# Optimization experiments

Hardware: AMD Instinct MI355X
Metric: run time of the kernel (lower is better)

Reference implementation:

```python
import jax, jax.numpy as jnp
import numpy as np

B, N, V, H, R, A, IN, K = 64, 512, 64, 512, 4, 18, 128, 32
EPS = 1e-8


def setup_inputs() -> dict:
    key = jax.random.key(0)
    ks = jax.random.split(key, 20)
    g = lambda i, shape, s=1.0: jax.random.normal(ks[i], shape, jnp.float32) * s
    u = lambda i, shape: jax.random.uniform(ks[i], shape, dtype=jnp.float32)
    cin = IN + R * V
    return dict(
        x=g(0, (B, IN)),
        h=g(1, (B, H), 0.1),
        c=g(2, (B, H), 0.1),
        memory=g(3, (B, N, V), 0.1),
        read_weights=u(4, (B, R, N)),
        write_weights=u(5, (B, N)),
        usage=u(6, (B, N)),
        link_matrix=u(7, (B, N, N)) * 0.01,
        precedence_weights=u(8, (B, N)),
        W_ih=g(9, (4 * H, cin), 0.05), W_hh=g(10, (4 * H, H), 0.05),
        b_ih=jnp.zeros(4 * H, jnp.float32), b_hh=jnp.zeros(4 * H, jnp.float32),
        W_read=g(11, (R, V + 4, H), 0.05), b_read=jnp.zeros((R, V + 4), jnp.float32),
        W_write=g(12, (3 * V + 3, H), 0.05), b_write=jnp.zeros(3 * V + 3, jnp.float32),
        W_pol=g(13, (A, H), 0.05), b_pol=jnp.zeros(A, jnp.float32),
        W_val=g(14, (1, H), 0.05), b_val=jnp.zeros(1, jnp.float32),
    )


def reference(x, h, c, memory, read_weights, write_weights, usage, link_matrix,
              precedence_weights, W_ih, W_hh, b_ih, b_hh, W_read, b_read,
              W_write, b_write, W_pol, b_pol, W_val, b_val):
    # ---- read heads (vectorized over R) ----
    ro = jnp.einsum('roh,bh->bro', W_read, h) + b_read            # [B,R,V+4]
    rkey = ro[..., :V]
    rbeta = jax.nn.softplus(ro[..., V])                           # [B,R]
    rpi = jax.nn.softmax(ro[..., V + 1:V + 4], axis=-1)           # backward/content/forward gates
    mem_norm = jnp.maximum(jnp.linalg.norm(memory, axis=-1), EPS)  # [B,N]
    key_norm = jnp.maximum(jnp.linalg.norm(rkey, axis=-1), EPS)    # [B,R]
    sim = jnp.einsum('bnv,brv->brn', memory, rkey) / (mem_norm[:, None, :] * key_norm[..., None])
    scores = rbeta[..., None] * sim                                # [B,R,N]
    kth = jax.lax.top_k(scores, K)[0][..., -1:]                    # sparse top-k mask
    cw = jax.nn.softmax(jnp.where(scores >= kth, scores, -jnp.inf), axis=-1)
    fw = jnp.einsum('bnm,brm->brn', link_matrix, read_weights)     # forward weighting L w
    bw = jnp.einsum('bmn,brm->brn', link_matrix, read_weights)     # backward weighting L^T w
    w_r = rpi[..., 0:1] * bw + rpi[..., 1:2] * cw + rpi[..., 2:3] * fw  # [B,R,N]
    rvec = jnp.einsum('brn,bnv->brv', w_r, memory).reshape(B, R * V)
    # ---- LSTM controller (torch LSTMCell gate order i,f,g,o) ----
    gates = jnp.concatenate([x, rvec], -1) @ W_ih.T + h @ W_hh.T + b_ih + b_hh
    i_g, f_g, g_g, o_g = jnp.split(gates, 4, axis=-1)
    c_new = jax.nn.sigmoid(f_g) * c + jax.nn.sigmoid(i_g) * jnp.tanh(g_g)
    h_new = jax.nn.sigmoid(o_g) * jnp.tanh(c_new)
    # ---- write head ----
    wo = h_new @ W_write.T + b_write                               # [B,3V+3]
    wkey = wo[:, :V]
    erase = jax.nn.sigmoid(wo[:, V:2 * V])
    add = jnp.tanh(wo[:, 2 * V:3 * V])
    wbeta = jax.nn.softplus(wo[:, 3 * V])
    g_a = jax.nn.sigmoid(wo[:, 3 * V + 1])
    g_w = jax.nn.sigmoid(wo[:, 3 * V + 2])
    wkey_norm = jnp.maximum(jnp.linalg.norm(wkey, axis=-1), EPS)
    wsim = jnp.einsum('bnv,bv->bn', memory, wkey) / (mem_norm * wkey_norm[:, None])
    cw_w = jax.nn.softmax(wbeta[:, None] * wsim, axis=-1)
    # allocation weighting from sorted usage (DNC Eq. 1)
    idx = jnp.argsort(usage, axis=-1)
    u_sorted = jnp.take_along_axis(usage, idx, -1)
    prod_prev = jnp.concatenate([jnp.ones((B, 1), usage.dtype), jnp.cumprod(u_sorted, -1)[:, :-1]], -1)
    a_sorted = (1.0 - u_sorted) * prod_prev
    alloc = jnp.take_along_axis(a_sorted, jnp.argsort(idx, -1), -1)
    write_w = g_w[:, None] * (g_a[:, None] * alloc + (1.0 - g_a)[:, None] * cw_w)  # [B,N]
    # ---- memory erase/add ----
    mem_new = memory * (1.0 - write_w[:, :, None] * erase[:, None, :]) + write_w[:, :, None] * add[:, None, :]
    # ---- usage (psi detached as in torch.no_grad) ----
    psi = jax.lax.stop_gradient(jnp.prod(1.0 - w_r, axis=1))
    usage_new = (usage + write_weights - usage * write_weights) * psi
    # ---- link matrix + precedence ----
    ws = jnp.sum(write_w, -1, keepdims=True)
    prec_new = (1.0 - ws) * precedence_weights + write_w
    decay = (1.0 - write_w[:, :, None]) * (1.0 - write_w[:, None, :])
    link_new = decay * link_matrix + write_w[:, :, None] * precedence_weights[:, None, :]
    link_new = link_new * (1.0 - jnp.eye(N, dtype=link_new.dtype))
    # ---- actor/critic heads ----
    logits = h_new @ W_pol.T + b_pol
    value = h_new @ W_val.T + b_val
    return (logits, value, h_new, c_new, mem_new, w_r, write_w, usage_new, link_new, prec_new)
```

## Files before the change

### kernel.cpp

```cpp
#include <hip/hip_runtime.h>
#include <math.h>

constexpr int Bb = 64, Nn = 512, Vv = 64, Hh = 512, Rr = 4, Aa = 18, INp = 128, KTOP = 32;
constexpr int CIN = 384;
constexpr int WOUT = 195;
#define EPSf 1e-8f

__device__ __forceinline__ float sigmoidf(float x){ return 1.f/(1.f+expf(-x)); }
__device__ __forceinline__ float softplusf(float x){ return (x>20.f)? x : log1pf(expf(x)); }
__device__ __forceinline__ float wave_reduce(float v){
  #pragma unroll
  for(int o=32;o>0;o>>=1) v += __shfl_down(v, o, 64);
  return v;
}
__device__ __forceinline__ unsigned f2ord(float f){
  unsigned u = __float_as_uint(f);
  return (u & 0x80000000u) ? ~u : (u | 0x80000000u);
}

__global__ void k_stage1(const float* __restrict__ link, const float* __restrict__ rw,
                         const float* __restrict__ Wr, const float* __restrict__ brd,
                         const float* __restrict__ h,
                         float* __restrict__ fw, float* __restrict__ bwpart,
                         float* __restrict__ rvec,
                         float* __restrict__ ro, float* __restrict__ rp) {
  __shared__ float bl[4][4][512];
  __shared__ float sh[512];
  __shared__ float sro[68];
  if (blockIdx.x < 512) {
    if (blockIdx.x < 64) rvec[blockIdx.x*256 + threadIdx.x] = 0.f;
    int b  = blockIdx.x >> 3;
    int ch = blockIdx.x & 7;
    int wv = threadIdx.x >> 6, lane = threadIdx.x & 63;
    const float* rwb = rw + b*Rr*Nn;
    float rwv[4][8];
    #pragma unroll
    for (int r = 0; r < 4; ++r)
      #pragma unroll
      for (int t = 0; t < 8; ++t) rwv[r][t] = rwb[r*512 + lane + 64*t];
    float bwacc[8][4] = {};
    const float* lb = link + (size_t)b*Nn*Nn;
    int n0 = ch*64 + wv*16;
    for (int i = 0; i < 16; ++i) {
      int n = n0 + i;
      float lk[8];
      #pragma unroll
      for (int t = 0; t < 8; ++t) lk[t] = lb[n*512 + lane + 64*t];
      float s0 = rwb[n], s1 = rwb[512+n], s2 = rwb[1024+n], s3 = rwb[1536+n];
      float f0=0,f1=0,f2=0,f3=0;
      #pragma unroll
      for (int t = 0; t < 8; ++t) {
        float lv = lk[t];
        f0 += lv*rwv[0][t]; f1 += lv*rwv[1][t]; f2 += lv*rwv[2][t]; f3 += lv*rwv[3][t];
        bwacc[t][0] += lv*s0; bwacc[t][1] += lv*s1; bwacc[t][2] += lv*s2; bwacc[t][3] += lv*s3;
      }
      f0 = wave_reduce(f0); f1 = wave_reduce(f1);
      f2 = wave_reduce(f2); f3 = wave_reduce(f3);
      if (lane == 0) {
        fw[(b*Rr+0)*Nn+n] = f0; fw[(b*Rr+1)*Nn+n] = f1;
        fw[(b*Rr+2)*Nn+n] = f2; fw[(b*Rr+3)*Nn+n] = f3;
      }
    }
    #pragma unroll
    for (int t = 0; t < 8; ++t)
      #pragma unroll
      for (int r = 0; r < 4; ++r) bl[wv][r][lane + 64*t] = bwacc[t][r];
    __syncthreads();
    int tid = threadIdx.x;
    #pragma unroll
    for (int q = 0; q < 8; ++q) {
      int idx = q*256 + tid;
      int r = idx >> 9, j = idx & 511;
      float v = bl[0][r][j] + bl[1][r][j] + bl[2][r][j] + bl[3][r][j];
      bwpart[((size_t)(ch*Bb + b)*Rr + r)*Nn + j] = v;
    }
  } else {
    int blk = blockIdx.x - 512;
    int b = blk >> 2, r = blk & 3;
    int wv = threadIdx.x >> 6, lane = threadIdx.x & 63;
    const float* hb = h + b*Hh;
    for (int i = threadIdx.x; i < 512; i += 256) sh[i] = hb[i];
    __syncthreads();
    const float* wbase = Wr + (size_t)(r*68)*Hh;
    for (int q = 0; q < 17; ++q) {
      int p = wv*17 + q;
      const float* wrow = wbase + (size_t)p*Hh;
      float acc = 0.f;
      #pragma unroll
      for (int t = 0; t < 8; ++t) { int k = lane + 64*t; acc += wrow[k]*sh[k]; }
      acc = wave_reduce(acc);
      if (lane == 0) sro[p] = acc + brd[r*68 + p];
    }
    __syncthreads();
    if (threadIdx.x < 68) ro[b*272 + r*68 + threadIdx.x] = sro[threadIdx.x];
    if (wv == 0) {
      float kv = sro[lane];
      float k2 = wave_reduce(kv*kv);
      if (lane == 0) {
        float rbeta = softplusf(sro[64]);
        float sc = rbeta / fmaxf(sqrtf(k2), EPSf);
        float e0 = sro[65], e1 = sro[66], e2 = sro[67];
        float mm = fmaxf(e0, fmaxf(e1, e2));
        float x0 = expf(e0-mm), x1 = expf(e1-mm), x2 = expf(e2-mm);
        float inv = 1.f/(x0+x1+x2);
        float* rpb = rp + (b*4 + r)*4;
        rpb[0] = sc; rpb[1] = x0*inv; rpb[2] = x1*inv; rpb[3] = x2*inv;
      }
    }
  }
}

__global__ void k_scores(const float* __restrict__ mem, const float* __restrict__ ro,
                         const float* __restrict__ rp, float* __restrict__ scores,
                         float* __restrict__ invmn) {
  int row = blockIdx.x*4 + (threadIdx.x>>6);
  int lane = threadIdx.x & 63;
  int b = row >> 9, n = row & 511;
  float m = mem[row*Vv + lane];
  const float* rob = ro + b*272;
  float v0 = m*m;
  float v1 = m * rob[lane];
  float v2 = m * rob[68  + lane];
  float v3 = m * rob[136 + lane];
  float v4 = m * rob[204 + lane];
  #pragma unroll
  for (int o = 32; o > 0; o >>= 1) {
    v0 += __shfl_down(v0,o,64); v1 += __shfl_down(v1,o,64);
    v2 += __shfl_down(v2,o,64); v3 += __shfl_down(v3,o,64);
    v4 += __shfl_down(v4,o,64);
  }
  if (lane == 0) {
    float im = 1.f / fmaxf(sqrtf(v0), EPSf);
    invmn[row] = im;
    const float* rpb = rp + b*16;
    scores[(b*4+0)*Nn+n] = rpb[0]  * v1 * im;
    scores[(b*4+1)*Nn+n] = rpb[4]  * v2 * im;
    scores[(b*4+2)*Nn+n] = rpb[8]  * v3 * im;
    scores[(b*4+3)*Nn+n] = rpb[12] * v4 * im;
  }
}

__global__ void k_topk_cw(const float* __restrict__ scores, float* __restrict__ cw) {
  __shared__ unsigned long long sk[512];
  __shared__ float sred[4];
  __shared__ float skv[2];
  int br = blockIdx.x, tid = threadIdx.x;
  float v0 = scores[br*Nn + tid], v1 = scores[br*Nn + tid + 256];
  unsigned long long k0 = ((unsigned long long)f2ord(v0) << 32) | (unsigned)(511 - tid);
  unsigned long long k1 = ((unsigned long long)f2ord(v1) << 32) | (unsigned)(255 - tid);
  sk[tid] = k0; sk[tid+256] = k1;
  __syncthreads();
  int c0 = 0, c1 = 0;
  #pragma unroll 8
  for (int j = 0; j < 512; ++j) {
    unsigned long long kj = sk[j];
    c0 += (kj > k0); c1 += (kj > k1);
  }
  if (c0 == KTOP-1) skv[0] = v0;
  if (c1 == KTOP-1) skv[0] = v1;
  if (c0 == 0) skv[1] = v0;
  if (c1 == 0) skv[1] = v1;
  __syncthreads();
  float kth = skv[0], mx = skv[1];
  float e0 = (v0 >= kth) ? expf(v0-mx) : 0.f;
  float e1 = (v1 >= kth) ? expf(v1-mx) : 0.f;
  float s = wave_reduce(e0+e1);
  if ((tid&63) == 0) sred[tid>>6] = s;
  __syncthreads();
  float inv = 1.f/(sred[0]+sred[1]+sred[2]+sred[3]);
  cw[br*Nn+tid]     = e0*inv;
  cw[br*Nn+tid+256] = e1*inv;
}

__global__ void k_wrrv(const float* __restrict__ bwpart, const float* __restrict__ cw,
                       const float* __restrict__ fw, const float* __restrict__ rp,
                       const float* __restrict__ usage, const float* __restrict__ wwt,
                       const float* __restrict__ mem,
                       float* __restrict__ out_wr, float* __restrict__ out_usage,
                       float* __restrict__ rvec) {
  __shared__ float swr[4][256];
  int b = blockIdx.x >> 1, ch = blockIdx.x & 1;
  int tid = threadIdx.x;
  int n = ch*256 + tid;
  int idx = b*Nn + n;
  float psi = 1.f;
  #pragma unroll
  for (int r = 0; r < 4; ++r) {
    int brr = b*4 + r;
    float bwv = 0.f;
    #pragma unroll
    for (int chh = 0; chh < 8; ++chh)
      bwv += bwpart[((size_t)(chh*Bb + b)*Rr + r)*Nn + n];
    const float* rpb = rp + brr*4;
    float w = rpb[1]*bwv + rpb[2]*cw[brr*Nn+n] + rpb[3]*fw[brr*Nn+n];
    out_wr[brr*Nn+n] = w;
    swr[r][tid] = w;
    psi *= (1.f - w);
  }
  float u = usage[idx], wt = wwt[idx];
  out_usage[idx] = (u + wt - u*wt) * psi;
  __syncthreads();
  int r = tid >> 6, v = tid & 63;
  const float* mb = mem + ((size_t)b*Nn + ch*256)*Vv + v;
  float acc = 0.f;
  #pragma unroll 4
  for (int t = 0; t < 256; ++t) acc += swr[r][t] * mb[t*Vv];
  atomicAdd(&rvec[(b*4+r)*Vv + v], acc);
}

__global__ void k_gates_lstm(const float* __restrict__ x, const float* __restrict__ rvec,
                             const float* __restrict__ h, const float* __restrict__ Wih,
                             const float* __restrict__ Whh, const float* __restrict__ bih,
                             const float* __restrict__ bhh, const float* __restrict__ c,
                             float* __restrict__ out_h, float* __restrict__ out_c) {
  int gid = blockIdx.x*4 + (threadIdx.x>>6);
  int lane = threadIdx.x & 63;
  int hh = gid >> 4;
  int bt = gid & 15;
  float acc[4][4] = {};
  #pragma unroll
  for (int t = 0; t < 6; ++t) {
    int k = lane + 64*t;
    float u[4], w[4];
    #pragma unroll
    for (int i = 0; i < 4; ++i) {
      int b = bt*4 + i;
      u[i] = (k < INp) ? x[b*INp + k] : rvec[b*(Rr*Vv) + k - INp];
      w[i] = Wih[(size_t)(i*Hh + hh)*CIN + k];
    }
    #pragma unroll
    for (int g = 0; g < 4; ++g)
      #pragma unroll
      for (int bb = 0; bb < 4; ++bb) acc[g][bb] += w[g]*u[bb];
  }
  #pragma unroll
  for (int t = 0; t < 8; ++t) {
    int k = lane + 64*t;
    float u[4], w[4];
    #pragma unroll
    for (int i = 0; i < 4; ++i) {
      u[i] = h[(bt*4+i)*Hh + k];
      w[i] = Whh[(size_t)(i*Hh + hh)*Hh + k];
    }
    #pragma unroll
    for (int g = 0; g < 4; ++g)
      #pragma unroll
      for (int bb = 0; bb < 4; ++bb) acc[g][bb] += w[g]*u[bb];
  }
  #pragma unroll
  for (int g = 0; g < 4; ++g)
    #pragma unroll
    for (int bb = 0; bb < 4; ++bb) acc[g][bb] = wave_reduce(acc[g][bb]);
  if (lane == 0) {
    float bsum[4];
    #pragma unroll
    for (int g = 0; g < 4; ++g) bsum[g] = bih[g*Hh + hh] + bhh[g*Hh + hh];
    #pragma unroll
    for (int bb = 0; bb < 4; ++bb) {
      int b = bt*4 + bb;
      float ig = sigmoidf(acc[0][bb] + bsum[0]);
      float fg = sigmoidf(acc[1][bb] + bsum[1]);
      float gg = tanhf   (acc[2][bb] + bsum[2]);
      float og = sigmoidf(acc[3][bb] + bsum[3]);
      float cn = fg * c[b*Hh + hh] + ig * gg;
      float hn = og * tanhf(cn);
      out_c[b*Hh + hh] = cn;
      out_h[b*Hh + hh] = hn;
    }
  }
}

__global__ void k_wopol(const float* __restrict__ hn, const float* __restrict__ Ww,
                        const float* __restrict__ bw_, const float* __restrict__ Wp,
                        const float* __restrict__ bp, const float* __restrict__ Wv,
                        const float* __restrict__ bv, float* __restrict__ wo,
                        float* __restrict__ out_logits, float* __restrict__ out_value) {
  int gid = blockIdx.x*4 + (threadIdx.x>>6);
  int lane = threadIdx.x & 63;
  int b = gid / 214, o = gid % 214;
  const float* wrow;
  if (o < WOUT) wrow = Ww + o*Hh;
  else if (o < WOUT + Aa) wrow = Wp + (o-WOUT)*Hh;
  else wrow = Wv;
  const float* hb = hn + b*Hh;
  float acc = 0.f;
  #pragma unroll
  for (int t = 0; t < 8; ++t) { int k = lane+64*t; acc += hb[k]*wrow[k]; }
  acc = wave_reduce(acc);
  if (lane == 0) {
    if (o < WOUT) wo[b*WOUT+o] = acc + bw_[o];
    else if (o < WOUT + Aa) out_logits[b*Aa + (o-WOUT)] = acc + bp[o-WOUT];
    else out_value[b] = acc + bv[0];
  }
}

__global__ void k_wsim(const float* __restrict__ mem, const float* __restrict__ wo,
                       const float* __restrict__ invmn, float* __restrict__ wsim) {
  int row = blockIdx.x*4 + (threadIdx.x>>6);
  int lane = threadIdx.x & 63;
  int b = row >> 9;
  const float* wob = wo + b*WOUT;
  float kv = wob[lane];
  float m = mem[row*Vv + lane];
  float v0 = m*kv, v1 = kv*kv;
  #pragma unroll
  for (int o = 32; o > 0; o >>= 1) {
    v0 += __shfl_down(v0,o,64); v1 += __shfl_down(v1,o,64);
  }
  if (lane == 0) {
    float wbeta = softplusf(wob[192]);
    wsim[row] = wbeta * v0 * invmn[row] / fmaxf(sqrtf(v1), EPSf);
  }
}

__global__ void k_alloc(const float* __restrict__ usage, const float* __restrict__ wo,
                        const float* __restrict__ wsim, const float* __restrict__ prec,
                        float* __restrict__ out_ww, float* __restrict__ out_prec) {
  __shared__ unsigned long long sk[512];
  __shared__ float su[512];
  __shared__ float cp[512];
  __shared__ float sred[8];
  int b = blockIdx.x, tid = threadIdx.x;
  int wv = tid >> 6, lane = tid & 63;
  float s0 = wsim[b*Nn+tid], s1 = wsim[b*Nn+tid+256];
  float u0 = usage[b*Nn+tid], u1 = usage[b*Nn+tid+256];
  unsigned long long k0 = ((unsigned long long)f2ord(u0) << 32) | (unsigned)tid;
  unsigned long long k1 = ((unsigned long long)f2ord(u1) << 32) | (unsigned)(tid+256);
  sk[tid] = k0; sk[tid+256] = k1;
  float mxl = fmaxf(s0, s1);
  #pragma unroll
  for (int o = 32; o > 0; o >>= 1) mxl = fmaxf(mxl, __shfl_down(mxl,o,64));
  if (lane == 0) sred[wv] = mxl;
  __syncthreads();
  float mx = fmaxf(fmaxf(sred[0],sred[1]), fmaxf(sred[2],sred[3]));
  float e0 = expf(s0-mx), e1 = expf(s1-mx);
  float ssum = wave_reduce(e0+e1);
  if (lane == 0) sred[4+wv] = ssum;
  int r0 = 0, r1 = 0;
  #pragma unroll 8
  for (int j = 0; j < 512; ++j) {
    unsigned long long kj = sk[j];
    r0 += (kj < k0); r1 += (kj < k1);
  }
  __syncthreads();
  float cinv = 1.f/(sred[4]+sred[5]+sred[6]+sred[7]);
  float c0 = e0*cinv, c1 = e1*cinv;
  su[r0] = u0; su[r1] = u1;
  __syncthreads();
  cp[tid] = su[tid]; cp[tid+256] = su[tid+256];
  __syncthreads();
  for (int d = 1; d < 512; d <<= 1) {
    float t0 = cp[tid]     * ((tid >= d)     ? cp[tid-d]     : 1.f);
    float t1 = cp[tid+256] * ((tid+256 >= d) ? cp[tid+256-d] : 1.f);
    __syncthreads();
    cp[tid] = t0; cp[tid+256] = t1;
    __syncthreads();
  }
  float pp0 = (r0 == 0) ? 1.f : cp[r0-1];
  float pp1 = (r1 == 0) ? 1.f : cp[r1-1];
  float a0 = (1.f-u0)*pp0, a1 = (1.f-u1)*pp1;
  float ga = sigmoidf(wo[b*WOUT+193]);
  float gw = sigmoidf(wo[b*WOUT+194]);
  float wv0 = gw * (ga*a0 + (1.f-ga)*c0);
  float wv1 = gw * (ga*a1 + (1.f-ga)*c1);
  out_ww[b*Nn+tid]     = wv0;
  out_ww[b*Nn+tid+256] = wv1;
  float ws_ = wave_reduce(wv0+wv1);
  if (lane == 0) sred[wv] = ws_;
  __syncthreads();
  float wsum = sred[0]+sred[1]+sred[2]+sred[3];
  out_prec[b*Nn+tid]     = (1.f-wsum)*prec[b*Nn+tid]     + wv0;
  out_prec[b*Nn+tid+256] = (1.f-wsum)*prec[b*Nn+tid+256] + wv1;
}

__global__ void k_memlink(const float* __restrict__ link, const float* __restrict__ ww,
                          const float* __restrict__ prec, const float* __restrict__ mem,
                          const float* __restrict__ wo, float* __restrict__ out_link,
                          float* __restrict__ out_mem) {
  int bid = blockIdx.x;
  if (bid < 16384) {
    int idx4 = bid*256 + threadIdx.x;
    int base = idx4*4;
    int b = base >> 18;
    int rem = base & 262143;
    int i = rem >> 9;
    int j0 = rem & 511;
    float wi = ww[b*Nn + i];
    float fi = 1.f - wi;
    float4 lv = *(const float4*)(link + base);
    float4 wj = *(const float4*)(ww + b*Nn + j0);
    float4 pj = *(const float4*)(prec + b*Nn + j0);
    float4 o;
    o.x = fi*(1.f-wj.x)*lv.x + wi*pj.x;
    o.y = fi*(1.f-wj.y)*lv.y + wi*pj.y;
    o.z = fi*(1.f-wj.z)*lv.z + wi*pj.z;
    o.w = fi*(1.f-wj.w)*lv.w + wi*pj.w;
    if (i >= j0 && i < j0+4) {
      if (i == j0) o.x = 0.f;
      else if (i == j0+1) o.y = 0.f;
      else if (i == j0+2) o.z = 0.f;
      else o.w = 0.f;
    }
    *(float4*)(out_link + base) = o;
  } else {
    int idx4 = (bid - 16384)*256 + threadIdx.x;
    int base = idx4*4;
    int b = base >> 15;
    int rem = base & 32767;
    int n = rem >> 6;
    int v0 = rem & 63;
    float w = ww[b*Nn + n];
    const float* wob = wo + b*WOUT;
    float4 m = *(const float4*)(mem + base);
    float4 o;
    float e, a;
    e = sigmoidf(wob[64+v0+0]); a = tanhf(wob[128+v0+0]); o.x = m.x*(1.f-w*e)+w*a;
    e = sigmoidf(wob[64+v0+1]); a = tanhf(wob[128+v0+1]); o.y = m.y*(1.f-w*e)+w*a;
    e = sigmoidf(wob[64+v0+2]); a = tanhf(wob[128+v0+2]); o.z = m.z*(1.f-w*e)+w*a;
    e = sigmoidf(wob[64+v0+3]); a = tanhf(wob[128+v0+3]); o.w = m.w*(1.f-w*e)+w*a;
    *(float4*)(out_mem + base) = o;
  }
}

extern "C" void kernel_launch(void* const* d_in, const int* in_sizes, int n_in,
                              void* d_out, int out_size, void* d_ws, size_t ws_size,
                              hipStream_t stream) {
  const float* x    = (const float*)d_in[0];
  const float* h    = (const float*)d_in[1];
  const float* c    = (const float*)d_in[2];
  const float* mem  = (const float*)d_in[3];
  const float* rw   = (const float*)d_in[4];
  const float* wwt  = (const float*)d_in[5];
  const float* usage= (const float*)d_in[6];
  const float* link = (const float*)d_in[7];
  const float* prec = (const float*)d_in[8];
  const float* Wih  = (const float*)d_in[9];
  const float* Whh  = (const float*)d_in[10];
  const float* bih  = (const float*)d_in[11];
  const float* bhh  = (const float*)d_in[12];
  const float* Wr   = (const float*)d_in[13];
  const float* br   = (const float*)d_in[14];
  const float* Ww   = (const float*)d_in[15];
  const float* bw_  = (const float*)d_in[16];
  const float* Wp   = (const float*)d_in[17];
  const float* bp   = (const float*)d_in[18];
  const float* Wv   = (const float*)d_in[19];
  const float* bv   = (const float*)d_in[20];

  float* out = (float*)d_out;
  float* o_logits = out + 0;
  float* o_value  = out + 1152;
  float* o_h      = out + 1216;
  float* o_c      = out + 33984;
  float* o_mem    = out + 66752;
  float* o_wr     = out + 2163904;
  float* o_ww     = out + 2294976;
  float* o_usage  = out + 2327744;
  float* o_link   = out + 2360512;
  float* o_prec   = out + 19137728;

  float* ws = (float*)d_ws;
  float* ws_ro     = ws;
  float* ws_rp     = ws + 17408;
  float* ws_sc     = ws + 18432;
  float* ws_cw     = ws + 149504;
  float* ws_fw     = ws + 280576;
  float* ws_bwpart = ws + 411648;
  float* ws_rvec   = ws + 1460224;
  float* ws_wo     = ws + 1476608;
  float* ws_wsim   = ws + 1489088;
  float* ws_invmn  = ws + 1521856;

  k_stage1     <<<dim3(768),       dim3(256), 0, stream>>>(link, rw, Wr, br, h, ws_fw, ws_bwpart, ws_rvec, ws_ro, ws_rp);
  k_scores     <<<dim3(Bb*Nn/4),   dim3(256), 0, stream>>>(mem, ws_ro, ws_rp, ws_sc, ws_invmn);
  k_topk_cw    <<<dim3(Bb*Rr),     dim3(256), 0, stream>>>(ws_sc, ws_cw);
  k_wrrv       <<<dim3(Bb*2),      dim3(256), 0, stream>>>(ws_bwpart, ws_cw, ws_fw, ws_rp, usage, wwt, mem, o_wr, o_usage, ws_rvec);
  k_gates_lstm <<<dim3(2048),      dim3(256), 0, stream>>>(x, ws_rvec, h, Wih, Whh, bih, bhh, c, o_h, o_c);
  k_wopol      <<<dim3(Bb*214/4),  dim3(256), 0, stream>>>(o_h, Ww, bw_, Wp, bp, Wv, bv, ws_wo, o_logits, o_value);
  k_wsim       <<<dim3(Bb*Nn/4),   dim3(256), 0, stream>>>(mem, ws_wo, ws_invmn, ws_wsim);
  k_alloc      <<<dim3(Bb),        dim3(256), 0, stream>>>(usage, ws_wo, ws_wsim, prec, o_ww, o_prec);
  k_memlink    <<<dim3(16384+2048),dim3(256), 0, stream>>>(link, o_ww, prec, mem, ws_wo, o_link, o_mem);
}
```

Measured before the change: 296.3 us.

## Fuse scores/top-k into stage1 and merge write-head kernels into one tail

Content-similarity scoring and sparse top-k softmax now run inside the read-head blocks of k_stage1, which compute the key and then score all 512 memory rows in place. The write-projection/policy/value matvec, the write similarity and the allocation logic are merged into a single per-batch k_tail kernel, cutting nine launches to five and dropping several intermediate buffers. The read-head matvec now processes four rows per pass, and the read-vector loop is unrolled further. The cost is that the tail matvec runs on only 64 blocks instead of thousands, and each thread reads whole memory rows with per-thread float4 strides, so parallelism in these phases drops.

After: 285.4 us. -3.6%, faster.

```diff
diff --git a/kernel.cpp b/kernel.cpp
--- a/kernel.cpp
+++ b/kernel.cpp
@@ -20,14 +20,13 @@
 
 __global__ void k_stage1(const float* __restrict__ link, const float* __restrict__ rw,
                          const float* __restrict__ Wr, const float* __restrict__ brd,
-                         const float* __restrict__ h,
+                         const float* __restrict__ h, const float* __restrict__ mem,
                          float* __restrict__ fw, float* __restrict__ bwpart,
-                         float* __restrict__ rvec,
-                         float* __restrict__ ro, float* __restrict__ rp) {
-  __shared__ float bl[4][4][512];
-  __shared__ float sh[512];
-  __shared__ float sro[68];
+                         float* __restrict__ rvec, float* __restrict__ rp,
+                         float* __restrict__ cw) {
+  __shared__ __align__(16) float smem[8192];
   if (blockIdx.x < 512) {
+    float (*bl)[4][512] = reinterpret_cast<float (*)[4][512]>(smem);
     if (blockIdx.x < 64) rvec[blockIdx.x*256 + threadIdx.x] = 0.f;
     int b  = blockIdx.x >> 3;
     int ch = blockIdx.x & 7;
@@ -75,24 +74,50 @@
       bwpart[((size_t)(ch*Bb + b)*Rr + r)*Nn + j] = v;
     }
   } else {
+    float* sh  = smem;
+    float* sro = smem + 512;
+    unsigned long long* sk = (unsigned long long*)(smem + 592);
+    float* sred = smem + 1616;
+    float* skv  = smem + 1620;
     int blk = blockIdx.x - 512;
     int b = blk >> 2, r = blk & 3;
-    int wv = threadIdx.x >> 6, lane = threadIdx.x & 63;
+    int tid = threadIdx.x;
+    int wv = tid >> 6, lane = tid & 63;
     const float* hb = h + b*Hh;
-    for (int i = threadIdx.x; i < 512; i += 256) sh[i] = hb[i];
+    for (int i = tid; i < 512; i += 256) sh[i] = hb[i];
     __syncthreads();
     const float* wbase = Wr + (size_t)(r*68)*Hh;
-    for (int q = 0; q < 17; ++q) {
-      int p = wv*17 + q;
-      const float* wrow = wbase + (size_t)p*Hh;
-      float acc = 0.f;
-      #pragma unroll
-      for (int t = 0; t < 8; ++t) { int k = lane + 64*t; acc += wrow[k]*sh[k]; }
-      acc = wave_reduce(acc);
-      if (lane == 0) sro[p] = acc + brd[r*68 + p];
-    }
-    __syncthreads();
-    if (threadIdx.x < 68) ro[b*272 + r*68 + threadIdx.x] = sro[threadIdx.x];
+    int pbase = wv*17;
+    #pragma unroll
+    for (int g = 0; g < 4; ++g) {
+      int p = pbase + g*4;
+      const float *w0 = wbase + (size_t)p*Hh, *w1 = w0 + Hh, *w2 = w1 + Hh, *w3 = w2 + Hh;
+      float a0=0,a1=0,a2=0,a3=0;
+      #pragma unroll
+      for (int t = 0; t < 8; ++t) {
+        int k = lane + 64*t; float hv = sh[k];
+        a0 += w0[k]*hv; a1 += w1[k]*hv; a2 += w2[k]*hv; a3 += w3[k]*hv;
+      }
+      #pragma unroll
+      for (int o = 32; o > 0; o >>= 1) {
+        a0 += __shfl_down(a0,o,64); a1 += __shfl_down(a1,o,64);
+        a2 += __shfl_down(a2,o,64); a3 += __shfl_down(a3,o,64);
+      }
+      if (lane == 0) {
+        sro[p]   = a0 + brd[r*68+p];   sro[p+1] = a1 + brd[r*68+p+1];
+        sro[p+2] = a2 + brd[r*68+p+2]; sro[p+3] = a3 + brd[r*68+p+3];
+      }
+    }
+    {
+      int p = pbase + 16;
+      const float* w0 = wbase + (size_t)p*Hh;
+      float a0 = 0.f;
+      #pragma unroll
+      for (int t = 0; t < 8; ++t) { int k = lane + 64*t; a0 += w0[k]*sh[k]; }
+      a0 = wave_reduce(a0);
+      if (lane == 0) sro[p] = a0 + brd[r*68+p];
+    }
+    __syncthreads();
     if (wv == 0) {
       float kv = sro[lane];
       float k2 = wave_reduce(kv*kv);
@@ -105,71 +130,61 @@
         float inv = 1.f/(x0+x1+x2);
         float* rpb = rp + (b*4 + r)*4;
         rpb[0] = sc; rpb[1] = x0*inv; rpb[2] = x1*inv; rpb[3] = x2*inv;
-      }
-    }
-  }
-}
-
-__global__ void k_scores(const float* __restrict__ mem, const float* __restrict__ ro,
-                         const float* __restrict__ rp, float* __restrict__ scores,
-                         float* __restrict__ invmn) {
-  int row = blockIdx.x*4 + (threadIdx.x>>6);
-  int lane = threadIdx.x & 63;
-  int b = row >> 9, n = row & 511;
-  float m = mem[row*Vv + lane];
-  const float* rob = ro + b*272;
-  float v0 = m*m;
-  float v1 = m * rob[lane];
-  float v2 = m * rob[68  + lane];
-  float v3 = m * rob[136 + lane];
-  float v4 = m * rob[204 + lane];
-  #pragma unroll
-  for (int o = 32; o > 0; o >>= 1) {
-    v0 += __shfl_down(v0,o,64); v1 += __shfl_down(v1,o,64);
-    v2 += __shfl_down(v2,o,64); v3 += __shfl_down(v3,o,64);
-    v4 += __shfl_down(v4,o,64);
-  }
-  if (lane == 0) {
-    float im = 1.f / fmaxf(sqrtf(v0), EPSf);
-    invmn[row] = im;
-    const float* rpb = rp + b*16;
-    scores[(b*4+0)*Nn+n] = rpb[0]  * v1 * im;
-    scores[(b*4+1)*Nn+n] = rpb[4]  * v2 * im;
-    scores[(b*4+2)*Nn+n] = rpb[8]  * v3 * im;
-    scores[(b*4+3)*Nn+n] = rpb[12] * v4 * im;
-  }
-}
-
-__global__ void k_topk_cw(const float* __restrict__ scores, float* __restrict__ cw) {
-  __shared__ unsigned long long sk[512];
-  __shared__ float sred[4];
-  __shared__ float skv[2];
-  int br = blockIdx.x, tid = threadIdx.x;
-  float v0 = scores[br*Nn + tid], v1 = scores[br*Nn + tid + 256];
-  unsigned long long k0 = ((unsigned long long)f2ord(v0) << 32) | (unsigned)(511 - tid);
-  unsigned long long k1 = ((unsigned long long)f2ord(v1) << 32) | (unsigned)(255 - tid);
-  sk[tid] = k0; sk[tid+256] = k1;
-  __syncthreads();
-  int c0 = 0, c1 = 0;
-  #pragma unroll 8
-  for (int j = 0; j < 512; ++j) {
-    unsigned long long kj = sk[j];
-    c0 += (kj > k0); c1 += (kj > k1);
-  }
-  if (c0 == KTOP-1) skv[0] = v0;
-  if (c1 == KTOP-1) skv[0] = v1;
-  if (c0 == 0) skv[1] = v0;
-  if (c1 == 0) skv[1] = v1;
-  __syncthreads();
-  float kth = skv[0], mx = skv[1];
-  float e0 = (v0 >= kth) ? expf(v0-mx) : 0.f;
-  float e1 = (v1 >= kth) ? expf(v1-mx) : 0.f;
-  float s = wave_reduce(e0+e1);
-  if ((tid&63) == 0) sred[tid>>6] = s;
-  __syncthreads();
-  float inv = 1.f/(sred[0]+sred[1]+sred[2]+sred[3]);
-  cw[br*Nn+tid]     = e0*inv;
-  cw[br*Nn+tid+256] = e1*inv;
+        sro[68] = sc;
+      }
+    }
+    __syncthreads();
+    float sc = sro[68];
+    const float4* key4 = (const float4*)sro;
+    float v0, v1;
+    {
+      const float4* m4 = (const float4*)(mem + ((size_t)(b*Nn + tid))*Vv);
+      float dot=0.f, nrm=0.f;
+      #pragma unroll
+      for (int i = 0; i < 16; ++i) {
+        float4 mv = m4[i]; float4 kk = key4[i];
+        dot += mv.x*kk.x + mv.y*kk.y + mv.z*kk.z + mv.w*kk.w;
+        nrm += mv.x*mv.x + mv.y*mv.y + mv.z*mv.z + mv.w*mv.w;
+      }
+      v0 = sc * dot / fmaxf(sqrtf(nrm), EPSf);
+    }
+    {
+      const float4* m4 = (const float4*)(mem + ((size_t)(b*Nn + tid + 256))*Vv);
+      float dot=0.f, nrm=0.f;
+      #pragma unroll
+      for (int i = 0; i < 16; ++i) {
+        float4 mv = m4[i]; float4 kk = key4[i];
+        dot += mv.x*kk.x + mv.y*kk.y + mv.z*kk.z + mv.w*kk.w;
+        nrm += mv.x*mv.x + mv.y*mv.y + mv.z*mv.z + mv.w*mv.w;
+      }
+      v1 = sc * dot / fmaxf(sqrtf(nrm), EPSf);
+    }
+    unsigned long long k0 = ((unsigned long long)f2ord(v0) << 32) | (unsigned)(511 - tid);
+    unsigned long long k1 = ((unsigned long long)f2ord(v1) << 32) | (unsigned)(255 - tid);
+    sk[tid] = k0; sk[tid+256] = k1;
+    __syncthreads();
+    int c0 = 0, c1 = 0;
+    #pragma unroll 8
+    for (int j = 0; j < 512; ++j) {
+      unsigned long long kj = sk[j];
+      c0 += (kj > k0); c1 += (kj > k1);
+    }
+    if (c0 == KTOP-1) skv[0] = v0;
+    if (c1 == KTOP-1) skv[0] = v1;
+    if (c0 == 0) skv[1] = v0;
+    if (c1 == 0) skv[1] = v1;
+    __syncthreads();
+    float kth = skv[0], mx = skv[1];
+    float e0 = (v0 >= kth) ? expf(v0-mx) : 0.f;
+    float e1 = (v1 >= kth) ? expf(v1-mx) : 0.f;
+    float s = wave_reduce(e0+e1);
+    if (lane == 0) sred[wv] = s;
+    __syncthreads();
+    float inv = 1.f/(sred[0]+sred[1]+sred[2]+sred[3]);
+    int brr = b*4 + r;
+    cw[brr*Nn+tid]     = e0*inv;
+    cw[brr*Nn+tid+256] = e1*inv;
+  }
 }
 
 __global__ void k_wrrv(const float* __restrict__ bwpart, const float* __restrict__ cw,
@@ -203,7 +218,7 @@
   int r = tid >> 6, v = tid & 63;
   const float* mb = mem + ((size_t)b*Nn + ch*256)*Vv + v;
   float acc = 0.f;
-  #pragma unroll 4
+  #pragma unroll 16
   for (int t = 0; t < 256; ++t) acc += swr[r][t] * mb[t*Vv];
   atomicAdd(&rvec[(b*4+r)*Vv + v], acc);
 }
@@ -270,59 +285,84 @@
   }
 }
 
-__global__ void k_wopol(const float* __restrict__ hn, const float* __restrict__ Ww,
-                        const float* __restrict__ bw_, const float* __restrict__ Wp,
-                        const float* __restrict__ bp, const float* __restrict__ Wv,
-                        const float* __restrict__ bv, float* __restrict__ wo,
-                        float* __restrict__ out_logits, float* __restrict__ out_value) {
-  int gid = blockIdx.x*4 + (threadIdx.x>>6);
-  int lane = threadIdx.x & 63;
-  int b = gid / 214, o = gid % 214;
-  const float* wrow;
-  if (o < WOUT) wrow = Ww + o*Hh;
-  else if (o < WOUT + Aa) wrow = Wp + (o-WOUT)*Hh;
-  else wrow = Wv;
-  const float* hb = hn + b*Hh;
-  float acc = 0.f;
-  #pragma unroll
-  for (int t = 0; t < 8; ++t) { int k = lane+64*t; acc += hb[k]*wrow[k]; }
-  acc = wave_reduce(acc);
-  if (lane == 0) {
-    if (o < WOUT) wo[b*WOUT+o] = acc + bw_[o];
-    else if (o < WOUT + Aa) out_logits[b*Aa + (o-WOUT)] = acc + bp[o-WOUT];
-    else out_value[b] = acc + bv[0];
-  }
-}
-
-__global__ void k_wsim(const float* __restrict__ mem, const float* __restrict__ wo,
-                       const float* __restrict__ invmn, float* __restrict__ wsim) {
-  int row = blockIdx.x*4 + (threadIdx.x>>6);
-  int lane = threadIdx.x & 63;
-  int b = row >> 9;
-  const float* wob = wo + b*WOUT;
-  float kv = wob[lane];
-  float m = mem[row*Vv + lane];
-  float v0 = m*kv, v1 = kv*kv;
-  #pragma unroll
-  for (int o = 32; o > 0; o >>= 1) {
-    v0 += __shfl_down(v0,o,64); v1 += __shfl_down(v1,o,64);
-  }
-  if (lane == 0) {
-    float wbeta = softplusf(wob[192]);
-    wsim[row] = wbeta * v0 * invmn[row] / fmaxf(sqrtf(v1), EPSf);
-  }
-}
-
-__global__ void k_alloc(const float* __restrict__ usage, const float* __restrict__ wo,
-                        const float* __restrict__ wsim, const float* __restrict__ prec,
-                        float* __restrict__ out_ww, float* __restrict__ out_prec) {
+__global__ void k_tail(const float* __restrict__ hn, const float* __restrict__ Ww,
+                       const float* __restrict__ bw_, const float* __restrict__ Wp,
+                       const float* __restrict__ bp, const float* __restrict__ Wv,
+                       const float* __restrict__ bv, const float* __restrict__ usage,
+                       const float* __restrict__ prec, const float* __restrict__ mem,
+                       float* __restrict__ wo, float* __restrict__ out_logits,
+                       float* __restrict__ out_value, float* __restrict__ out_ww,
+                       float* __restrict__ out_prec) {
+  __shared__ __align__(16) float sh[512];
+  __shared__ __align__(16) float swo[200];
   __shared__ unsigned long long sk[512];
   __shared__ float su[512];
   __shared__ float cp[512];
   __shared__ float sred[8];
   int b = blockIdx.x, tid = threadIdx.x;
   int wv = tid >> 6, lane = tid & 63;
-  float s0 = wsim[b*Nn+tid], s1 = wsim[b*Nn+tid+256];
+  const float* hb = hn + b*Hh;
+  for (int i = tid; i < 512; i += 256) sh[i] = hb[i];
+  __syncthreads();
+  int dbeg = wv*54, dend = (dbeg + 54 < 214) ? dbeg + 54 : 214;
+  for (int p = dbeg; p < dend; p += 4) {
+    int d1 = (p+1 < 213) ? p+1 : 213, d2 = (p+2 < 213) ? p+2 : 213, d3 = (p+3 < 213) ? p+3 : 213;
+    const float* w0 = (p  < WOUT) ? Ww + (size_t)p *Hh : ((p  < WOUT+Aa) ? Wp + (size_t)(p -WOUT)*Hh : Wv);
+    const float* w1 = (d1 < WOUT) ? Ww + (size_t)d1*Hh : ((d1 < WOUT+Aa) ? Wp + (size_t)(d1-WOUT)*Hh : Wv);
+    const float* w2 = (d2 < WOUT) ? Ww + (size_t)d2*Hh : ((d2 < WOUT+Aa) ? Wp + (size_t)(d2-WOUT)*Hh : Wv);
+    const float* w3 = (d3 < WOUT) ? Ww + (size_t)d3*Hh : ((d3 < WOUT+Aa) ? Wp + (size_t)(d3-WOUT)*Hh : Wv);
+    float a0=0,a1=0,a2=0,a3=0;
+    #pragma unroll
+    for (int t = 0; t < 8; ++t) {
+      int k = lane + 64*t; float hv = sh[k];
+      a0 += w0[k]*hv; a1 += w1[k]*hv; a2 += w2[k]*hv; a3 += w3[k]*hv;
+    }
+    #pragma unroll
+    for (int o = 32; o > 0; o >>= 1) {
+      a0 += __shfl_down(a0,o,64); a1 += __shfl_down(a1,o,64);
+      a2 += __shfl_down(a2,o,64); a3 += __shfl_down(a3,o,64);
+    }
+    if (lane == 0) {
+      float av[4] = {a0,a1,a2,a3};
+      #pragma unroll
+      for (int i = 0; i < 4; ++i) {
+        int d = p + i;
+        if (d >= dend) break;
+        float a = av[i];
+        if (d < WOUT)          { float vv = a + bw_[d]; swo[d] = vv; wo[b*WOUT+d] = vv; }
+        else if (d < WOUT+Aa)  { out_logits[b*Aa + (d-WOUT)] = a + bp[d-WOUT]; }
+        else                   { out_value[b] = a + bv[0]; }
+      }
+    }
+  }
+  __syncthreads();
+  float wbeta = softplusf(swo[192]);
+  const float4* key4 = (const float4*)swo;
+  float s0, s1;
+  {
+    const float4* m4 = (const float4*)(mem + ((size_t)(b*Nn + tid))*Vv);
+    float dot=0.f, nrm=0.f, kn=0.f;
+    #pragma unroll
+    for (int i = 0; i < 16; ++i) {
+      float4 mv = m4[i]; float4 kk = key4[i];
+      dot += mv.x*kk.x + mv.y*kk.y + mv.z*kk.z + mv.w*kk.w;
+      nrm += mv.x*mv.x + mv.y*mv.y + mv.z*mv.z + mv.w*mv.w;
+      kn  += kk.x*kk.x + kk.y*kk.y + kk.z*kk.z + kk.w*kk.w;
+    }
+    s0 = wbeta * dot / (fmaxf(sqrtf(nrm), EPSf) * fmaxf(sqrtf(kn), EPSf));
+  }
+  {
+    const float4* m4 = (const float4*)(mem + ((size_t)(b*Nn + tid + 256))*Vv);
+    float dot=0.f, nrm=0.f, kn=0.f;
+    #pragma unroll
+    for (int i = 0; i < 16; ++i) {
+      float4 mv = m4[i]; float4 kk = key4[i];
+      dot += mv.x*kk.x + mv.y*kk.y + mv.z*kk.z + mv.w*kk.w;
+      nrm += mv.x*mv.x + mv.y*mv.y + mv.z*mv.z + mv.w*mv.w;
+      kn  += kk.x*kk.x + kk.y*kk.y + kk.z*kk.z + kk.w*kk.w;
+    }
+    s1 = wbeta * dot / (fmaxf(sqrtf(nrm), EPSf) * fmaxf(sqrtf(kn), EPSf));
+  }
   float u0 = usage[b*Nn+tid], u1 = usage[b*Nn+tid+256];
   unsigned long long k0 = ((unsigned long long)f2ord(u0) << 32) | (unsigned)tid;
   unsigned long long k1 = ((unsigned long long)f2ord(u1) << 32) | (unsigned)(tid+256);
@@ -359,8 +399,8 @@
   float pp0 = (r0 == 0) ? 1.f : cp[r0-1];
   float pp1 = (r1 == 0) ? 1.f : cp[r1-1];
   float a0 = (1.f-u0)*pp0, a1 = (1.f-u1)*pp1;
-  float ga = sigmoidf(wo[b*WOUT+193]);
-  float gw = sigmoidf(wo[b*WOUT+194]);
+  float ga = sigmoidf(swo[193]);
+  float gw = sigmoidf(swo[194]);
   float wv0 = gw * (ga*a0 + (1.f-ga)*c0);
   float wv1 = gw * (ga*a1 + (1.f-ga)*c1);
   out_ww[b*Nn+tid]     = wv0;
@@ -460,24 +500,16 @@
   float* o_prec   = out + 19137728;
 
   float* ws = (float*)d_ws;
-  float* ws_ro     = ws;
-  float* ws_rp     = ws + 17408;
-  float* ws_sc     = ws + 18432;
-  float* ws_cw     = ws + 149504;
-  float* ws_fw     = ws + 280576;
-  float* ws_bwpart = ws + 411648;
-  float* ws_rvec   = ws + 1460224;
-  float* ws_wo     = ws + 1476608;
-  float* ws_wsim   = ws + 1489088;
-  float* ws_invmn  = ws + 1521856;
-
-  k_stage1     <<<dim3(768),       dim3(256), 0, stream>>>(link, rw, Wr, br, h, ws_fw, ws_bwpart, ws_rvec, ws_ro, ws_rp);
-  k_scores     <<<dim3(Bb*Nn/4),   dim3(256), 0, stream>>>(mem, ws_ro, ws_rp, ws_sc, ws_invmn);
-  k_topk_cw    <<<dim3(Bb*Rr),     dim3(256), 0, stream>>>(ws_sc, ws_cw);
-  k_wrrv       <<<dim3(Bb*2),      dim3(256), 0, stream>>>(ws_bwpart, ws_cw, ws_fw, ws_rp, usage, wwt, mem, o_wr, o_usage, ws_rvec);
-  k_gates_lstm <<<dim3(2048),      dim3(256), 0, stream>>>(x, ws_rvec, h, Wih, Whh, bih, bhh, c, o_h, o_c);
-  k_wopol      <<<dim3(Bb*214/4),  dim3(256), 0, stream>>>(o_h, Ww, bw_, Wp, bp, Wv, bv, ws_wo, o_logits, o_value);
-  k_wsim       <<<dim3(Bb*Nn/4),   dim3(256), 0, stream>>>(mem, ws_wo, ws_invmn, ws_wsim);
-  k_alloc      <<<dim3(Bb),        dim3(256), 0, stream>>>(usage, ws_wo, ws_wsim, prec, o_ww, o_prec);
-  k_memlink    <<<dim3(16384+2048),dim3(256), 0, stream>>>(link, o_ww, prec, mem, ws_wo, o_link, o_mem);
-}
+  float* ws_rp     = ws;
+  float* ws_cw     = ws + 1024;
+  float* ws_fw     = ws + 132096;
+  float* ws_bwpart = ws + 263168;
+  float* ws_rvec   = ws + 1311744;
+  float* ws_wo     = ws + 1328128;
+
+  k_stage1     <<<dim3(768),        dim3(256), 0, stream>>>(link, rw, Wr, br, h, mem, ws_fw, ws_bwpart, ws_rvec, ws_rp, ws_cw);
+  k_wrrv       <<<dim3(Bb*2),       dim3(256), 0, stream>>>(ws_bwpart, ws_cw, ws_fw, ws_rp, usage, wwt, mem, o_wr, o_usage, ws_rvec);
+  k_gates_lstm <<<dim3(2048),       dim3(256), 0, stream>>>(x, ws_rvec, h, Wih, Whh, bih, bhh, c, o_h, o_c);
+  k_tail       <<<dim3(Bb),         dim3(256), 0, stream>>>(o_h, Ww, bw_, Wp, bp, Wv, bv, usage, prec, mem, ws_wo, o_logits, o_value, o_ww, o_prec);
+  k_memlink    <<<dim3(16384+2048), dim3(256), 0, stream>>>(link, o_ww, prec, mem, ws_wo, o_link, o_mem);
+}
```
